# Performance work log

Hardware: AMD Instinct MI355X
Metric: run time of the kernel (lower is better)

Reference implementation:

```python
import jax, jax.numpy as jnp
import numpy as np

MARGIN = 1.0
EPS = 1e-05
B = 8192
D = 128
NUM_CLASSES = 256


def setup_inputs() -> dict:
    key = jax.random.key(0)
    k1, k2 = jax.random.split(key)
    feature = jax.random.normal(k1, (B, D), dtype=jnp.float32)
    label = jax.random.randint(k2, (B,), 0, NUM_CLASSES, dtype=jnp.int32)
    return {"feature": feature, "label": label}


def reference(feature, label):
    # Pairwise Euclidean distance matrix: ||x_i||^2 + ||x_j||^2 - 2 x_i.x_j + eps, then sqrt
    sq = jnp.sum(feature * feature, axis=1, keepdims=True)  # [B, 1]
    dist = jnp.sqrt(jnp.maximum(sq + sq.T - 2.0 * (feature @ feature.T) + EPS, 0.0))  # [B, B]

    same = label[:, None] == label[None, :]  # [B, B] bool, includes self on diagonal
    inf = jnp.array(jnp.inf, dtype=dist.dtype)

    # Original sorts each row and takes same[1]: the SECOND smallest same-label distance
    # (the smallest is the anchor itself, distance sqrt(eps)).
    d_same = jnp.where(same, dist, inf)
    two_smallest = -jax.lax.top_k(-d_same, 2)[0]  # [B, 2], ascending smallest two
    pos = two_smallest[:, 1]  # nearest positive excluding self

    # diff.min(): hardest (closest) negative per row
    neg = jnp.min(jnp.where(same, inf, dist), axis=1)

    hinge = jnp.maximum(MARGIN + pos - neg, 0.0)
    return jnp.mean(hinge)
```

## Files before the change

kernel.cpp:

```cpp
#include <hip/hip_runtime.h>
#include <math.h>


#define BN 8192
#define MARGIN_F 1.0f
#define EPS_F 1e-5f

typedef __attribute__((ext_vector_type(8))) short short8;
typedef __attribute__((ext_vector_type(4))) float floatx4;

__device__ __forceinline__ unsigned short bf16_rne(float x, float& r) {
    unsigned u = __float_as_uint(x);
    u += 0x7FFF + ((u >> 16) & 1);
    unsigned short h = (unsigned short)(u >> 16);
    r = __uint_as_float(((unsigned)h) << 16);
    return h;
}

__global__ __launch_bounds__(256) void prep_kernel(const float* __restrict__ f,
                                                   short8* __restrict__ fbT,
                                                   float* __restrict__ sq,
                                                   float* __restrict__ g_acc,
                                                   unsigned* __restrict__ counter) {
    int gid = blockIdx.x * 256 + threadIdx.x;
    if (gid == 0) { *g_acc = 0.f; *counter = 0u; }
    int row = gid >> 2, part = gid & 3;
    const float4* f4 = (const float4*)f + (size_t)row * 32 + part * 8;
    float s = 0.f;
#pragma unroll
    for (int cc = 0; cc < 4; ++cc) {
        float4 v0 = f4[cc * 2], v1 = f4[cc * 2 + 1];
        float r0, r1, r2, r3, r4, r5, r6, r7;
        short8 o;
        o[0] = (short)bf16_rne(v0.x, r0);
        o[1] = (short)bf16_rne(v0.y, r1);
        o[2] = (short)bf16_rne(v0.z, r2);
        o[3] = (short)bf16_rne(v0.w, r3);
        o[4] = (short)bf16_rne(v1.x, r4);
        o[5] = (short)bf16_rne(v1.y, r5);
        o[6] = (short)bf16_rne(v1.z, r6);
        o[7] = (short)bf16_rne(v1.w, r7);
        fbT[(size_t)(part * 4 + cc) * BN + row] = o;
        s += r0 * r0 + r1 * r1 + r2 * r2 + r3 * r3 +
             r4 * r4 + r5 * r5 + r6 * r6 + r7 * r7;
    }
    s += __shfl_xor(s, 1, 4);
    s += __shfl_xor(s, 2, 4);
    if (part == 0) sq[row] = s;
}

__global__ __launch_bounds__(256, 3) void work_kernel(const short8* __restrict__ fbT,
                                                      const int* __restrict__ lbl,
                                                      const float* __restrict__ sq,
                                                      float* __restrict__ part,
                                                      float* __restrict__ pos_d2) {
    const int t = threadIdx.x;
    const int lane = t & 63;
    const int wv = t >> 6;
    const int q = lane >> 4, c = lane & 15;
    const int bid = blockIdx.x;

    if (bid >= 512) {
        __shared__ int midx[256];
        __shared__ int cnt;
        const int cls = bid - 512;
        if (t == 0) cnt = 0;
        __syncthreads();
        for (int r = t; r < BN; r += 256) {
            if (lbl[r] == cls) {
                int p = atomicAdd(&cnt, 1);
                if (p < 256) midx[p] = r;
            }
        }
        __syncthreads();
        int n = cnt < 256 ? cnt : 256;
        if (n == 0) return;
        if (t < 256 && t >= n) midx[t] = midx[0];
        __syncthreads();

        const int ng = (n + 15) >> 4;
        for (int ig = wv; ig < ng; ig += 4) {
            short8 a[4];
            int arow = midx[ig * 16 + c];
#pragma unroll
            for (int ks = 0; ks < 4; ++ks)
                a[ks] = fbT[(size_t)(ks * 4 + q) * BN + arow];
            float s1[4], s2[4];
#pragma unroll
            for (int rg = 0; rg < 4; ++rg) { s1[rg] = INFINITY; s2[rg] = INFINITY; }

            for (int s = 0; s < ng; ++s) {
                int jslot = s * 16 + c;
                int jrow = midx[jslot];
                short8 b[4];
#pragma unroll
                for (int ks = 0; ks < 4; ++ks)
                    b[ks] = fbT[(size_t)(ks * 4 + q) * BN + jrow];
                float sj = sq[jrow];
                bool valid = (jslot < n);

                floatx4 acc = (floatx4)0.f;
#pragma unroll
                for (int ks = 0; ks < 4; ++ks)
                    acc = __builtin_amdgcn_mfma_f32_16x16x32_bf16(a[ks], b[ks], acc, 0, 0, 0);
#pragma unroll
                for (int rg = 0; rg < 4; ++rg) {
                    float v = fmaf(-2.0f, acc[rg], sj);
                    float vs = valid ? v : INFINITY;
                    s2[rg] = fminf(s2[rg], fmaxf(s1[rg], vs));
                    s1[rg] = fminf(s1[rg], vs);
                }
            }
#pragma unroll
            for (int m = 1; m < 16; m <<= 1) {
#pragma unroll
                for (int rg = 0; rg < 4; ++rg) {
                    float o1 = __shfl_xor(s1[rg], m, 16);
                    float o2 = __shfl_xor(s2[rg], m, 16);
                    float lo = fminf(s1[rg], o1);
                    float hi = fminf(fmaxf(s1[rg], o1), fminf(s2[rg], o2));
                    s1[rg] = lo; s2[rg] = hi;
                }
            }
            if (c == 0) {
#pragma unroll
                for (int rg = 0; rg < 4; ++rg) {
                    int islot = ig * 16 + q * 4 + rg;
                    if (islot < n) {
                        int row = midx[islot];
                        pos_d2[row] = sq[row] + s2[rg];
                    }
                }
            }
        }
        return;
    }

    const int i0 = (bid & 63) * 128 + wv * 32;
    const int g = bid >> 6;
    const int jb = g * 1024;

    short8 a[2][4];
#pragma unroll
    for (int mf = 0; mf < 2; ++mf) {
        int row = i0 + mf * 16 + c;
#pragma unroll
        for (int ks = 0; ks < 4; ++ks)
            a[mf][ks] = fbT[(size_t)(ks * 4 + q) * BN + row];
    }
    int li[2][4];
#pragma unroll
    for (int mf = 0; mf < 2; ++mf)
#pragma unroll
        for (int rg = 0; rg < 4; ++rg)
            li[mf][rg] = lbl[i0 + mf * 16 + q * 4 + rg];

    float n1[2][4];
#pragma unroll
    for (int mf = 0; mf < 2; ++mf)
#pragma unroll
        for (int rg = 0; rg < 4; ++rg) n1[mf][rg] = INFINITY;

#pragma unroll 2
    for (int jt = 0; jt < 16; ++jt) {
        const int j0 = jb + jt * 64;

        int ljv[4]; float sjv[4];
#pragma unroll
        for (int nf = 0; nf < 4; ++nf) {
            int jc = j0 + nf * 16 + c;
            ljv[nf] = lbl[jc];
            sjv[nf] = sq[jc];
        }

        floatx4 acc[2][4];
#pragma unroll
        for (int mf = 0; mf < 2; ++mf)
#pragma unroll
            for (int nf = 0; nf < 4; ++nf) acc[mf][nf] = (floatx4)0.f;

#pragma unroll
        for (int ks = 0; ks < 4; ++ks) {
            short8 b[4];
#pragma unroll
            for (int nf = 0; nf < 4; ++nf)
                b[nf] = fbT[(size_t)(ks * 4 + q) * BN + j0 + nf * 16 + c];
#pragma unroll
            for (int mf = 0; mf < 2; ++mf)
#pragma unroll
                for (int nf = 0; nf < 4; ++nf)
                    acc[mf][nf] = __builtin_amdgcn_mfma_f32_16x16x32_bf16(
                        a[mf][ks], b[nf], acc[mf][nf], 0, 0, 0);
        }

#pragma unroll
        for (int nf = 0; nf < 4; ++nf) {
#pragma unroll
            for (int mf = 0; mf < 2; ++mf)
#pragma unroll
                for (int rg = 0; rg < 4; ++rg) {
                    float v = fmaf(-2.0f, acc[mf][nf][rg], sjv[nf]);
                    float vd = (li[mf][rg] == ljv[nf]) ? INFINITY : v;
                    n1[mf][rg] = fminf(n1[mf][rg], vd);
                }
        }
    }

#pragma unroll
    for (int m = 1; m < 16; m <<= 1) {
#pragma unroll
        for (int mf = 0; mf < 2; ++mf)
#pragma unroll
            for (int rg = 0; rg < 4; ++rg)
                n1[mf][rg] = fminf(n1[mf][rg], __shfl_xor(n1[mf][rg], m, 16));
    }
    if (c == 0) {
#pragma unroll
        for (int mf = 0; mf < 2; ++mf)
#pragma unroll
            for (int rg = 0; rg < 4; ++rg)
                part[g * BN + i0 + mf * 16 + q * 4 + rg] = n1[mf][rg];
    }
}

__global__ __launch_bounds__(128) void merge_kernel(const float* __restrict__ part,
                                                    const float* __restrict__ sq,
                                                    const float* __restrict__ pos_d2,
                                                    float* __restrict__ g_acc,
                                                    unsigned* __restrict__ counter,
                                                    float* __restrict__ out) {
    int r = blockIdx.x * 128 + threadIdx.x;
    float n = INFINITY;
#pragma unroll
    for (int k = 0; k < 8; ++k) n = fminf(n, part[k * BN + r]);
    float si = sq[r];
    float pos = sqrtf(fmaxf(pos_d2[r] + EPS_F, 0.f));
    float neg = sqrtf(fmaxf(si + n + EPS_F, 0.f));
    float h = fmaxf(MARGIN_F + pos - neg, 0.f);
    __shared__ float red[2];
#pragma unroll
    for (int m = 32; m >= 1; m >>= 1) h += __shfl_down(h, m, 64);
    if ((threadIdx.x & 63) == 0) red[threadIdx.x >> 6] = h;
    __syncthreads();
    if (threadIdx.x == 0) {
        atomicAdd(g_acc, red[0] + red[1]);
        __threadfence();
        unsigned old = atomicAdd(counter, 1u);
        if (old == 63u) {
            float tot = atomicAdd(g_acc, 0.0f);
            out[0] = tot / (float)BN;
        }
    }
}

extern "C" void kernel_launch(void* const* d_in, const int* in_sizes, int n_in,
                              void* d_out, int out_size, void* d_ws, size_t ws_size,
                              hipStream_t stream) {
    const float* f = (const float*)d_in[0];
    const int* lbl = (const int*)d_in[1];
    char* ws = (char*)d_ws;
    float* sq = (float*)ws;
    short8* fbT = (short8*)(ws + 32768);
    float* part = (float*)(ws + 32768 + 2097152);
    float* pos_d2 = (float*)(ws + 32768 + 2097152 + 262144);
    float* g_acc = (float*)(ws + 32768 + 2097152 + 262144 + 32768);
    unsigned* counter = (unsigned*)(g_acc + 1);
    float* out = (float*)d_out;

    prep_kernel<<<128, 256, 0, stream>>>(f, fbT, sq, g_acc, counter);
    work_kernel<<<768, 256, 0, stream>>>(fbT, lbl, sq, part, pos_d2);
    merge_kernel<<<64, 128, 0, stream>>>(part, sq, pos_d2, g_acc, counter, out);
}
```

Baseline: 87.96 us.

## Split column range into 16 groups, pack label with norm, widen prep

The work kernel now splits the column dimension into 16 chunks of 512 instead of 8 chunks of 1024, doubling the negative-search blocks to 1024 and raising the launch-bounds occupancy hint to 4. Labels and squared norms are packed into one float2 array so each column tile needs a single 8-byte load instead of two 4-byte loads. The prep kernel uses 8 threads per row to spread the conversion over more blocks. The cost is twice as many partial minima for the merge kernel to read and a larger workspace.

```diff
diff --git a/kernel.cpp b/kernel.cpp
--- a/kernel.cpp
+++ b/kernel.cpp
@@ -18,17 +18,18 @@
 }
 
 __global__ __launch_bounds__(256) void prep_kernel(const float* __restrict__ f,
+                                                   const int* __restrict__ lbl,
                                                    short8* __restrict__ fbT,
-                                                   float* __restrict__ sq,
+                                                   float2* __restrict__ lsq,
                                                    float* __restrict__ g_acc,
                                                    unsigned* __restrict__ counter) {
     int gid = blockIdx.x * 256 + threadIdx.x;
     if (gid == 0) { *g_acc = 0.f; *counter = 0u; }
-    int row = gid >> 2, part = gid & 3;
-    const float4* f4 = (const float4*)f + (size_t)row * 32 + part * 8;
+    int row = gid >> 3, part = gid & 7;
+    const float4* f4 = (const float4*)f + (size_t)row * 32 + part * 4;
     float s = 0.f;
 #pragma unroll
-    for (int cc = 0; cc < 4; ++cc) {
+    for (int cc = 0; cc < 2; ++cc) {
         float4 v0 = f4[cc * 2], v1 = f4[cc * 2 + 1];
         float r0, r1, r2, r3, r4, r5, r6, r7;
         short8 o;
@@ -40,18 +41,24 @@
         o[5] = (short)bf16_rne(v1.y, r5);
         o[6] = (short)bf16_rne(v1.z, r6);
         o[7] = (short)bf16_rne(v1.w, r7);
-        fbT[(size_t)(part * 4 + cc) * BN + row] = o;
+        fbT[(size_t)(part * 2 + cc) * BN + row] = o;
         s += r0 * r0 + r1 * r1 + r2 * r2 + r3 * r3 +
              r4 * r4 + r5 * r5 + r6 * r6 + r7 * r7;
     }
-    s += __shfl_xor(s, 1, 4);
-    s += __shfl_xor(s, 2, 4);
-    if (part == 0) sq[row] = s;
-}
-
-__global__ __launch_bounds__(256, 3) void work_kernel(const short8* __restrict__ fbT,
+    s += __shfl_xor(s, 1, 8);
+    s += __shfl_xor(s, 2, 8);
+    s += __shfl_xor(s, 4, 8);
+    if (part == 0) {
+        float2 p;
+        p.x = s;
+        p.y = __int_as_float(lbl[row]);
+        lsq[row] = p;
+    }
+}
+
+__global__ __launch_bounds__(256, 4) void work_kernel(const short8* __restrict__ fbT,
                                                       const int* __restrict__ lbl,
-                                                      const float* __restrict__ sq,
+                                                      const float2* __restrict__ lsq,
                                                       float* __restrict__ part,
                                                       float* __restrict__ pos_d2) {
     const int t = threadIdx.x;
@@ -60,10 +67,10 @@
     const int q = lane >> 4, c = lane & 15;
     const int bid = blockIdx.x;
 
-    if (bid >= 512) {
+    if (bid >= 1024) {
         __shared__ int midx[256];
         __shared__ int cnt;
-        const int cls = bid - 512;
+        const int cls = bid - 1024;
         if (t == 0) cnt = 0;
         __syncthreads();
         for (int r = t; r < BN; r += 256) {
@@ -96,7 +103,7 @@
 #pragma unroll
                 for (int ks = 0; ks < 4; ++ks)
                     b[ks] = fbT[(size_t)(ks * 4 + q) * BN + jrow];
-                float sj = sq[jrow];
+                float sj = lsq[jrow].x;
                 bool valid = (jslot < n);
 
                 floatx4 acc = (floatx4)0.f;
@@ -128,7 +135,7 @@
                     int islot = ig * 16 + q * 4 + rg;
                     if (islot < n) {
                         int row = midx[islot];
-                        pos_d2[row] = sq[row] + s2[rg];
+                        pos_d2[row] = lsq[row].x + s2[rg];
                     }
                 }
             }
@@ -138,7 +145,7 @@
 
     const int i0 = (bid & 63) * 128 + wv * 32;
     const int g = bid >> 6;
-    const int jb = g * 1024;
+    const int jb = g * 512;
 
     short8 a[2][4];
 #pragma unroll
@@ -153,7 +160,7 @@
     for (int mf = 0; mf < 2; ++mf)
 #pragma unroll
         for (int rg = 0; rg < 4; ++rg)
-            li[mf][rg] = lbl[i0 + mf * 16 + q * 4 + rg];
+            li[mf][rg] = __float_as_int(lsq[i0 + mf * 16 + q * 4 + rg].y);
 
     float n1[2][4];
 #pragma unroll
@@ -162,15 +169,15 @@
         for (int rg = 0; rg < 4; ++rg) n1[mf][rg] = INFINITY;
 
 #pragma unroll 2
-    for (int jt = 0; jt < 16; ++jt) {
+    for (int jt = 0; jt < 8; ++jt) {
         const int j0 = jb + jt * 64;
 
         int ljv[4]; float sjv[4];
 #pragma unroll
         for (int nf = 0; nf < 4; ++nf) {
-            int jc = j0 + nf * 16 + c;
-            ljv[nf] = lbl[jc];
-            sjv[nf] = sq[jc];
+            float2 p = lsq[j0 + nf * 16 + c];
+            sjv[nf] = p.x;
+            ljv[nf] = __float_as_int(p.y);
         }
 
         floatx4 acc[2][4];
@@ -224,7 +231,7 @@
 }
 
 __global__ __launch_bounds__(128) void merge_kernel(const float* __restrict__ part,
-                                                    const float* __restrict__ sq,
+                                                    const float2* __restrict__ lsq,
                                                     const float* __restrict__ pos_d2,
                                                     float* __restrict__ g_acc,
                                                     unsigned* __restrict__ counter,
@@ -232,8 +239,8 @@
     int r = blockIdx.x * 128 + threadIdx.x;
     float n = INFINITY;
 #pragma unroll
-    for (int k = 0; k < 8; ++k) n = fminf(n, part[k * BN + r]);
-    float si = sq[r];
+    for (int k = 0; k < 16; ++k) n = fminf(n, part[k * BN + r]);
+    float si = lsq[r].x;
     float pos = sqrtf(fmaxf(pos_d2[r] + EPS_F, 0.f));
     float neg = sqrtf(fmaxf(si + n + EPS_F, 0.f));
     float h = fmaxf(MARGIN_F + pos - neg, 0.f);
@@ -259,15 +266,15 @@
     const float* f = (const float*)d_in[0];
     const int* lbl = (const int*)d_in[1];
     char* ws = (char*)d_ws;
-    float* sq = (float*)ws;
-    short8* fbT = (short8*)(ws + 32768);
-    float* part = (float*)(ws + 32768 + 2097152);
-    float* pos_d2 = (float*)(ws + 32768 + 2097152 + 262144);
-    float* g_acc = (float*)(ws + 32768 + 2097152 + 262144 + 32768);
+    float2* lsq = (float2*)ws;
+    short8* fbT = (short8*)(ws + 65536);
+    float* part = (float*)(ws + 65536 + 2097152);
+    float* pos_d2 = (float*)(ws + 65536 + 2097152 + 524288);
+    float* g_acc = (float*)(ws + 65536 + 2097152 + 524288 + 32768);
     unsigned* counter = (unsigned*)(g_acc + 1);
     float* out = (float*)d_out;
 
-    prep_kernel<<<128, 256, 0, stream>>>(f, fbT, sq, g_acc, counter);
-    work_kernel<<<768, 256, 0, stream>>>(fbT, lbl, sq, part, pos_d2);
-    merge_kernel<<<64, 128, 0, stream>>>(part, sq, pos_d2, g_acc, counter, out);
-}
+    prep_kernel<<<256, 256, 0, stream>>>(f, lbl, fbT, lsq, g_acc, counter);
+    work_kernel<<<1280, 256, 0, stream>>>(fbT, lbl, lsq, part, pos_d2);
+    merge_kernel<<<64, 128, 0, stream>>>(part, lsq, pos_d2, g_acc, counter, out);
+}
```

Result: slower. 93.58 us (+6.4%).
